# Performance work log

Hardware: AMD Instinct MI355X
Metric: run time of the kernel (lower is better)

The kernel has to match this reference:

```python
import jax, jax.numpy as jnp
import numpy as np

DIM = 256
NUM_HEADS = 8
HEAD_DIM = DIM // NUM_HEADS


def setup_inputs() -> dict:
    key = jax.random.key(0)
    k_x, k_wq, k_bq, k_wp, k_bp = jax.random.split(key, 5)
    B, C, H, W = 2, DIM, 48, 48
    x = jax.random.normal(k_x, (B, C, H, W), dtype=jnp.float32)
    # 1x1 convs are pointwise matmuls: store weights as [out, in]
    w_qkv = jax.random.normal(k_wq, (3 * C, C), dtype=jnp.float32) * (1.0 / np.sqrt(C))
    b_qkv = jax.random.normal(k_bq, (3 * C,), dtype=jnp.float32) * 0.01
    w_proj = jax.random.normal(k_wp, (C, C), dtype=jnp.float32) * (1.0 / np.sqrt(C))
    b_proj = jax.random.normal(k_bp, (C,), dtype=jnp.float32) * 0.01
    return {"x": x, "w_qkv": w_qkv, "b_qkv": b_qkv, "w_proj": w_proj, "b_proj": b_proj}


def reference(x, w_qkv, b_qkv, w_proj, b_proj):
    B, C, H, W = x.shape
    N = H * W
    # qkv 1x1 conv -> pointwise channel matmul
    qkv = jnp.einsum('bchw,oc->bohw', x, w_qkv) + b_qkv[None, :, None, None]
    q, k, v = jnp.split(qkv, 3, axis=1)  # each [B, C, H, W]
    q = q.reshape(B, NUM_HEADS, HEAD_DIM, N)
    k = k.reshape(B, NUM_HEADS, HEAD_DIM, N)
    v = v.reshape(B, NUM_HEADS, HEAD_DIM, N)
    scale = 1.0 / (HEAD_DIM ** 0.5)
    attn = jnp.einsum('bhdn,bhdm->bhnm', q, k) * scale  # [B, H, N, N]
    attn = jax.nn.softmax(attn, axis=-1)
    out = jnp.einsum('bhnm,bhdm->bhdn', attn, v)  # [B, heads, head_dim, N]
    out = out.reshape(B, C, H, W)
    out = jnp.einsum('bchw,oc->bohw', out, w_proj) + b_proj[None, :, None, None]
    return out + x
```

## Files before the change

### kernel.cpp

```cpp
#include <hip/hip_runtime.h>
#include <math.h>

#define C_DIM 256
#define NH 8
#define HD 32
#define BATCH 2
#define NPIX 2304
#define TK 64
#define KP 72

typedef __attribute__((ext_vector_type(8))) short bf16x8;
typedef __attribute__((ext_vector_type(4))) float f32x4;

__device__ __forceinline__ unsigned short f2b(float f) {
    union { float f; unsigned int u; } c; c.f = f;
    unsigned int u = c.u + 0x7FFFu + ((c.u >> 16) & 1u);
    return (unsigned short)(u >> 16);
}

__device__ __forceinline__ unsigned int pk2(float lo, float hi) {
    union { float f; unsigned int u; } a, b;
    a.f = lo; b.f = hi;
    return __builtin_amdgcn_perm(b.u + 0x8000u, a.u + 0x8000u, 0x07060302u);
}

__global__ __launch_bounds__(256) void qkv_gemm(
        const float* __restrict__ x, const float* __restrict__ w,
        const float* __restrict__ bias,
        unsigned short* __restrict__ Qg, unsigned short* __restrict__ Kg,
        unsigned short* __restrict__ Vg)
{
    __shared__ unsigned short a_s[128][KP];
    __shared__ unsigned short b_s[128][KP];

    const int tid  = threadIdx.x;
    const int wv   = tid >> 6;
    const int lane = tid & 63;
    const int l15  = lane & 15;
    const int quad = lane >> 4;
    const int n0   = blockIdx.x * 128;
    const int my   = blockIdx.y;
    const int b    = blockIdx.z;
    const float* xb = x + (size_t)b * C_DIM * NPIX;

    f32x4 acc[8][2];
    #pragma unroll
    for (int i = 0; i < 8; ++i) { acc[i][0] = (f32x4){0,0,0,0}; acc[i][1] = (f32x4){0,0,0,0}; }

    const int ak = (tid & 15) * 4, ai = tid >> 4;
    const int bn = tid & 63,       bk = (tid >> 6) * 16;

    for (int kk = 0; kk < C_DIM; kk += 64) {
        #pragma unroll
        for (int p = 0; p < 8; ++p) {
            const int i = p * 16 + ai;
            const float4 w4 = *(const float4*)(w + (size_t)(my * 128 + i) * C_DIM + kk + ak);
            *(uint2*)&a_s[i][ak] = make_uint2(pk2(w4.x, w4.y), pk2(w4.z, w4.w));
        }
        #pragma unroll
        for (int half = 0; half < 2; ++half) {
            const int n = half * 64 + bn;
            const float* xc = xb + (size_t)(kk + bk) * NPIX + n0 + n;
            #pragma unroll
            for (int t = 0; t < 4; ++t) {
                const float v0 = xc[(size_t)(t * 4 + 0) * NPIX];
                const float v1 = xc[(size_t)(t * 4 + 1) * NPIX];
                const float v2 = xc[(size_t)(t * 4 + 2) * NPIX];
                const float v3 = xc[(size_t)(t * 4 + 3) * NPIX];
                *(uint2*)&b_s[n][bk + t * 4] = make_uint2(pk2(v0, v1), pk2(v2, v3));
            }
        }
        __syncthreads();

        #pragma unroll
        for (int ks = 0; ks < 2; ++ks) {
            bf16x8 bfr[2];
            bfr[0] = *(const bf16x8*)&b_s[wv * 32 + l15][ks * 32 + quad * 8];
            bfr[1] = *(const bf16x8*)&b_s[wv * 32 + 16 + l15][ks * 32 + quad * 8];
            #pragma unroll
            for (int mt = 0; mt < 8; ++mt) {
                const bf16x8 af = *(const bf16x8*)&a_s[mt * 16 + l15][ks * 32 + quad * 8];
                acc[mt][0] = __builtin_amdgcn_mfma_f32_16x16x32_bf16(af, bfr[0], acc[mt][0], 0, 0, 0);
                acc[mt][1] = __builtin_amdgcn_mfma_f32_16x16x32_bf16(af, bfr[1], acc[mt][1], 0, 0, 0);
            }
        }
        __syncthreads();
    }

    const int which = my >> 1;
    #pragma unroll
    for (int mt = 0; mt < 8; ++mt) {
        const int m0 = my * 128 + mt * 16 + quad * 4;
        const float4 b4 = *(const float4*)(bias + m0);
        const int h  = (m0 >> 5) & 7;
        const int d0 = m0 & 31;
        const int bh = b * NH + h;
        #pragma unroll
        for (int nt = 0; nt < 2; ++nt) {
            const int n = n0 + wv * 32 + nt * 16 + l15;
            float v0 = acc[mt][nt][0] + b4.x;
            float v1 = acc[mt][nt][1] + b4.y;
            float v2 = acc[mt][nt][2] + b4.z;
            float v3 = acc[mt][nt][3] + b4.w;
            if (which == 0) {
                const float s = 0.17677669529663687f;
                v0 *= s; v1 *= s; v2 *= s; v3 *= s;
                *(uint2*)&Qg[((size_t)bh * NPIX + n) * HD + d0] =
                    make_uint2(pk2(v0, v1), pk2(v2, v3));
            } else if (which == 1) {
                *(uint2*)&Kg[((size_t)bh * NPIX + n) * HD + d0] =
                    make_uint2(pk2(v0, v1), pk2(v2, v3));
            } else {
                unsigned short* vp = Vg + (size_t)bh * HD * NPIX + (size_t)d0 * NPIX + n;
                vp[0]        = f2b(v0);
                vp[NPIX]     = f2b(v1);
                vp[2 * NPIX] = f2b(v2);
                vp[3 * NPIX] = f2b(v3);
            }
        }
    }
}

#define NT (NPIX / TK)

__global__ __launch_bounds__(256) void attn_kernel(
        const unsigned short* __restrict__ Qg, const unsigned short* __restrict__ Kg,
        const unsigned short* __restrict__ Vg, float* __restrict__ Ot)
{
    __shared__ unsigned short k_s[2][TK][40];
    __shared__ unsigned short v_s[2][HD][76];
    __shared__ unsigned short p_s[4][16][76];
    __shared__ float o_s[HD][68];

    const int tid  = threadIdx.x;
    const int wv   = tid >> 6;
    const int lane = tid & 63;
    const int l15  = lane & 15;
    const int quad = lane >> 4;
    const int bh   = blockIdx.y;
    const int q0   = blockIdx.x * 64;

    const unsigned short* Qh = Qg + (size_t)bh * NPIX * HD;
    const unsigned short* Kh = Kg + (size_t)bh * NPIX * HD;
    const unsigned short* Vh = Vg + (size_t)bh * HD * NPIX;

    const bf16x8 q_frag = *(const bf16x8*)(Qh + (size_t)(q0 + wv * 16 + l15) * HD + quad * 8);

    const int kr = tid >> 2, kc = (tid & 3) * 8;
    const int vd = tid >> 3, vc = (tid & 7) * 8;

    uint4 kreg = *(const uint4*)(Kh + (size_t)kr * HD + kc);
    uint4 vreg = *(const uint4*)(Vh + (size_t)vd * NPIX + vc);
    *(uint4*)&k_s[0][kr][kc] = kreg;
    *(uint4*)&v_s[0][vd][vc] = vreg;

    f32x4 o0 = {0.f, 0.f, 0.f, 0.f};
    f32x4 o1 = {0.f, 0.f, 0.f, 0.f};
    float lsum = 0.f;

    for (int t = 0; t < NT; ++t) {
        const int cur = t & 1;
        if (t + 1 < NT) {
            const int k0 = (t + 1) * TK;
            kreg = *(const uint4*)(Kh + (size_t)(k0 + kr) * HD + kc);
            vreg = *(const uint4*)(Vh + (size_t)vd * NPIX + k0 + vc);
        }
        __syncthreads();

        f32x4 s[4];
        #pragma unroll
        for (int kg = 0; kg < 4; ++kg) {
            const bf16x8 kf = *(const bf16x8*)&k_s[cur][kg * 16 + l15][quad * 8];
            s[kg] = __builtin_amdgcn_mfma_f32_16x16x32_bf16(kf, q_frag,
                        (f32x4){0.f, 0.f, 0.f, 0.f}, 0, 0, 0);
        }

        #pragma unroll
        for (int kg = 0; kg < 4; ++kg) {
            const float p0 = __expf(s[kg][0]);
            const float p1 = __expf(s[kg][1]);
            const float p2 = __expf(s[kg][2]);
            const float p3 = __expf(s[kg][3]);
            lsum += (p0 + p1) + (p2 + p3);
            *(uint2*)&p_s[wv][l15][kg * 16 + quad * 4] =
                make_uint2(pk2(p0, p1), pk2(p2, p3));
        }

        #pragma unroll
        for (int kc2 = 0; kc2 < 2; ++kc2) {
            const bf16x8 pf  = *(const bf16x8*)&p_s[wv][l15][kc2 * 32 + quad * 8];
            const bf16x8 vf0 = *(const bf16x8*)&v_s[cur][l15][kc2 * 32 + quad * 8];
            const bf16x8 vf1 = *(const bf16x8*)&v_s[cur][16 + l15][kc2 * 32 + quad * 8];
            o0 = __builtin_amdgcn_mfma_f32_16x16x32_bf16(vf0, pf, o0, 0, 0, 0);
            o1 = __builtin_amdgcn_mfma_f32_16x16x32_bf16(vf1, pf, o1, 0, 0, 0);
        }

        if (t + 1 < NT) {
            *(uint4*)&k_s[cur ^ 1][kr][kc] = kreg;
            *(uint4*)&v_s[cur ^ 1][vd][vc] = vreg;
        }
    }

    lsum += __shfl_xor(lsum, 16, 64);
    lsum += __shfl_xor(lsum, 32, 64);
    const float inv = 1.f / lsum;

    #pragma unroll
    for (int r = 0; r < 4; ++r) {
        o_s[quad * 4 + r][wv * 16 + l15]      = o0[r] * inv;
        o_s[16 + quad * 4 + r][wv * 16 + l15] = o1[r] * inv;
    }
    __syncthreads();
    const int row = tid >> 3, col = (tid & 7) * 8;
    const int b = bh >> 3, h = bh & 7;
    float* op = Ot + ((size_t)b * C_DIM + h * HD + row) * NPIX + q0 + col;
    *(float4*)op       = *(float4*)&o_s[row][col];
    *((float4*)op + 1) = *(float4*)&o_s[row][col + 4];
}

__global__ __launch_bounds__(256) void proj_gemm(
        const float* __restrict__ A, const float* __restrict__ w,
        const float* __restrict__ bias, const float* __restrict__ x,
        float* __restrict__ out)
{
    __shared__ unsigned short a_s[64][KP];
    __shared__ unsigned short b_s[128][KP];

    const int tid  = threadIdx.x;
    const int wv   = tid >> 6;
    const int lane = tid & 63;
    const int l15  = lane & 15;
    const int quad = lane >> 4;
    const int n0   = blockIdx.x * 128;
    const int my   = blockIdx.y;
    const int b    = blockIdx.z;
    const float* Ab = A + (size_t)b * C_DIM * NPIX;

    f32x4 acc[4][2];
    #pragma unroll
    for (int i = 0; i < 4; ++i) { acc[i][0] = (f32x4){0,0,0,0}; acc[i][1] = (f32x4){0,0,0,0}; }

    const int ak = (tid & 15) * 4, ai = tid >> 4;
    const int bn = tid & 63,       bk = (tid >> 6) * 16;

    for (int kk = 0; kk < C_DIM; kk += 64) {
        #pragma unroll
        for (int p = 0; p < 4; ++p) {
            const int i = p * 16 + ai;
            const float4 w4 = *(const float4*)(w + (size_t)(my * 64 + i) * C_DIM + kk + ak);
            *(uint2*)&a_s[i][ak] = make_uint2(pk2(w4.x, w4.y), pk2(w4.z, w4.w));
        }
        #pragma unroll
        for (int half = 0; half < 2; ++half) {
            const int n = half * 64 + bn;
            const float* xc = Ab + (size_t)(kk + bk) * NPIX + n0 + n;
            #pragma unroll
            for (int t = 0; t < 4; ++t) {
                const float v0 = xc[(size_t)(t * 4 + 0) * NPIX];
                const float v1 = xc[(size_t)(t * 4 + 1) * NPIX];
                const float v2 = xc[(size_t)(t * 4 + 2) * NPIX];
                const float v3 = xc[(size_t)(t * 4 + 3) * NPIX];
                *(uint2*)&b_s[n][bk + t * 4] = make_uint2(pk2(v0, v1), pk2(v2, v3));
            }
        }
        __syncthreads();

        #pragma unroll
        for (int ks = 0; ks < 2; ++ks) {
            bf16x8 bfr[2];
            bfr[0] = *(const bf16x8*)&b_s[wv * 32 + l15][ks * 32 + quad * 8];
            bfr[1] = *(const bf16x8*)&b_s[wv * 32 + 16 + l15][ks * 32 + quad * 8];
            #pragma unroll
            for (int mt = 0; mt < 4; ++mt) {
                const bf16x8 af = *(const bf16x8*)&a_s[mt * 16 + l15][ks * 32 + quad * 8];
                acc[mt][0] = __builtin_amdgcn_mfma_f32_16x16x32_bf16(af, bfr[0], acc[mt][0], 0, 0, 0);
                acc[mt][1] = __builtin_amdgcn_mfma_f32_16x16x32_bf16(af, bfr[1], acc[mt][1], 0, 0, 0);
            }
        }
        __syncthreads();
    }

    #pragma unroll
    for (int mt = 0; mt < 4; ++mt) {
        const int m0 = my * 64 + mt * 16 + quad * 4;
        const float4 b4 = *(const float4*)(bias + m0);
        #pragma unroll
        for (int nt = 0; nt < 2; ++nt) {
            const int n = n0 + wv * 32 + nt * 16 + l15;
            const size_t base = ((size_t)b * C_DIM + m0) * NPIX + n;
            out[base]            = acc[mt][nt][0] + b4.x + x[base];
            out[base + NPIX]     = acc[mt][nt][1] + b4.y + x[base + NPIX];
            out[base + 2 * NPIX] = acc[mt][nt][2] + b4.z + x[base + 2 * NPIX];
            out[base + 3 * NPIX] = acc[mt][nt][3] + b4.w + x[base + 3 * NPIX];
        }
    }
}

extern "C" void kernel_launch(void* const* d_in, const int* in_sizes, int n_in,
                              void* d_out, int out_size, void* d_ws, size_t ws_size,
                              hipStream_t stream)
{
    const float* x      = (const float*)d_in[0];
    const float* w_qkv  = (const float*)d_in[1];
    const float* b_qkv  = (const float*)d_in[2];
    const float* w_proj = (const float*)d_in[3];
    const float* b_proj = (const float*)d_in[4];
    float* out = (float*)d_out;

    const size_t TSZ = (size_t)BATCH * NH * NPIX * HD;
    unsigned short* Qg = (unsigned short*)d_ws;
    unsigned short* Kg = Qg + TSZ;
    unsigned short* Vg = Qg + 2 * TSZ;
    float* Ot = (float*)(Qg + 3 * TSZ);

    qkv_gemm<<<dim3(18, 6, 2), 256, 0, stream>>>(x, w_qkv, b_qkv, Qg, Kg, Vg);
    attn_kernel<<<dim3(36, 16), 256, 0, stream>>>(Qg, Kg, Vg, Ot);
    proj_gemm<<<dim3(18, 4, 2), 256, 0, stream>>>(Ot, w_proj, b_proj, x, out);
}
```

Measured before the change: 121.8 us.

## Shrink GEMM tiles and double-buffer LDS with register prefetch in both 1x1-conv GEMMs

Both pointwise GEMM kernels move to smaller output tiles (64x64 for qkv, 32x64 for proj), which gives 4x more blocks so more CUs are occupied. The global loads for the next K slice are prefetched into registers and written to a second LDS buffer while MFMAs run on the current buffer, leaving one barrier per step instead of two. The attention grid is transposed so that consecutive blocks cover different heads. Smaller tiles mean less reuse per loaded element and more redundant weight and activation traffic.

```diff
diff --git a/kernel.cpp b/kernel.cpp
--- a/kernel.cpp
+++ b/kernel.cpp
@@ -30,93 +30,108 @@
         unsigned short* __restrict__ Qg, unsigned short* __restrict__ Kg,
         unsigned short* __restrict__ Vg)
 {
-    __shared__ unsigned short a_s[128][KP];
-    __shared__ unsigned short b_s[128][KP];
+    __shared__ unsigned short a_s[2][64][KP];
+    __shared__ unsigned short b_s[2][64][KP];
 
     const int tid  = threadIdx.x;
     const int wv   = tid >> 6;
     const int lane = tid & 63;
     const int l15  = lane & 15;
     const int quad = lane >> 4;
-    const int n0   = blockIdx.x * 128;
+    const int n0   = blockIdx.x * 64;
     const int my   = blockIdx.y;
     const int b    = blockIdx.z;
     const float* xb = x + (size_t)b * C_DIM * NPIX;
 
-    f32x4 acc[8][2];
-    #pragma unroll
-    for (int i = 0; i < 8; ++i) { acc[i][0] = (f32x4){0,0,0,0}; acc[i][1] = (f32x4){0,0,0,0}; }
+    f32x4 acc[4];
+    #pragma unroll
+    for (int i = 0; i < 4; ++i) acc[i] = (f32x4){0.f, 0.f, 0.f, 0.f};
 
     const int ak = (tid & 15) * 4, ai = tid >> 4;
     const int bn = tid & 63,       bk = (tid >> 6) * 16;
 
-    for (int kk = 0; kk < C_DIM; kk += 64) {
-        #pragma unroll
-        for (int p = 0; p < 8; ++p) {
-            const int i = p * 16 + ai;
-            const float4 w4 = *(const float4*)(w + (size_t)(my * 128 + i) * C_DIM + kk + ak);
-            *(uint2*)&a_s[i][ak] = make_uint2(pk2(w4.x, w4.y), pk2(w4.z, w4.w));
-        }
-        #pragma unroll
-        for (int half = 0; half < 2; ++half) {
-            const int n = half * 64 + bn;
-            const float* xc = xb + (size_t)(kk + bk) * NPIX + n0 + n;
-            #pragma unroll
-            for (int t = 0; t < 4; ++t) {
-                const float v0 = xc[(size_t)(t * 4 + 0) * NPIX];
-                const float v1 = xc[(size_t)(t * 4 + 1) * NPIX];
-                const float v2 = xc[(size_t)(t * 4 + 2) * NPIX];
-                const float v3 = xc[(size_t)(t * 4 + 3) * NPIX];
-                *(uint2*)&b_s[n][bk + t * 4] = make_uint2(pk2(v0, v1), pk2(v2, v3));
+    float4 aw[4];
+    float  bw[16];
+
+    #pragma unroll
+    for (int p = 0; p < 4; ++p)
+        aw[p] = *(const float4*)(w + (size_t)(my * 64 + p * 16 + ai) * C_DIM + ak);
+    {
+        const float* xc = xb + (size_t)bk * NPIX + n0 + bn;
+        #pragma unroll
+        for (int t = 0; t < 16; ++t) bw[t] = xc[(size_t)t * NPIX];
+    }
+    #pragma unroll
+    for (int p = 0; p < 4; ++p)
+        *(uint2*)&a_s[0][p * 16 + ai][ak] =
+            make_uint2(pk2(aw[p].x, aw[p].y), pk2(aw[p].z, aw[p].w));
+    #pragma unroll
+    for (int t = 0; t < 4; ++t)
+        *(uint2*)&b_s[0][bn][bk + t * 4] =
+            make_uint2(pk2(bw[t*4], bw[t*4+1]), pk2(bw[t*4+2], bw[t*4+3]));
+
+    #pragma unroll
+    for (int step = 0; step < 4; ++step) {
+        const int cur = step & 1;
+        if (step < 3) {
+            const int kk = (step + 1) * 64;
+            #pragma unroll
+            for (int p = 0; p < 4; ++p)
+                aw[p] = *(const float4*)(w + (size_t)(my * 64 + p * 16 + ai) * C_DIM + kk + ak);
+            const float* xc = xb + (size_t)(kk + bk) * NPIX + n0 + bn;
+            #pragma unroll
+            for (int t = 0; t < 16; ++t) bw[t] = xc[(size_t)t * NPIX];
+        }
+        __syncthreads();
+
+        #pragma unroll
+        for (int ks = 0; ks < 2; ++ks) {
+            const bf16x8 bfr = *(const bf16x8*)&b_s[cur][wv * 16 + l15][ks * 32 + quad * 8];
+            #pragma unroll
+            for (int mt = 0; mt < 4; ++mt) {
+                const bf16x8 af = *(const bf16x8*)&a_s[cur][mt * 16 + l15][ks * 32 + quad * 8];
+                acc[mt] = __builtin_amdgcn_mfma_f32_16x16x32_bf16(af, bfr, acc[mt], 0, 0, 0);
             }
         }
-        __syncthreads();
-
-        #pragma unroll
-        for (int ks = 0; ks < 2; ++ks) {
-            bf16x8 bfr[2];
-            bfr[0] = *(const bf16x8*)&b_s[wv * 32 + l15][ks * 32 + quad * 8];
-            bfr[1] = *(const bf16x8*)&b_s[wv * 32 + 16 + l15][ks * 32 + quad * 8];
-            #pragma unroll
-            for (int mt = 0; mt < 8; ++mt) {
-                const bf16x8 af = *(const bf16x8*)&a_s[mt * 16 + l15][ks * 32 + quad * 8];
-                acc[mt][0] = __builtin_amdgcn_mfma_f32_16x16x32_bf16(af, bfr[0], acc[mt][0], 0, 0, 0);
-                acc[mt][1] = __builtin_amdgcn_mfma_f32_16x16x32_bf16(af, bfr[1], acc[mt][1], 0, 0, 0);
-            }
-        }
-        __syncthreads();
-    }
-
-    const int which = my >> 1;
-    #pragma unroll
-    for (int mt = 0; mt < 8; ++mt) {
-        const int m0 = my * 128 + mt * 16 + quad * 4;
+        if (step < 3) {
+            #pragma unroll
+            for (int p = 0; p < 4; ++p)
+                *(uint2*)&a_s[cur ^ 1][p * 16 + ai][ak] =
+                    make_uint2(pk2(aw[p].x, aw[p].y), pk2(aw[p].z, aw[p].w));
+            #pragma unroll
+            for (int t = 0; t < 4; ++t)
+                *(uint2*)&b_s[cur ^ 1][bn][bk + t * 4] =
+                    make_uint2(pk2(bw[t*4], bw[t*4+1]), pk2(bw[t*4+2], bw[t*4+3]));
+        }
+    }
+
+    const int which = my >> 2;
+    #pragma unroll
+    for (int mt = 0; mt < 4; ++mt) {
+        const int m0 = my * 64 + mt * 16 + quad * 4;
         const float4 b4 = *(const float4*)(bias + m0);
         const int h  = (m0 >> 5) & 7;
         const int d0 = m0 & 31;
         const int bh = b * NH + h;
-        #pragma unroll
-        for (int nt = 0; nt < 2; ++nt) {
-            const int n = n0 + wv * 32 + nt * 16 + l15;
-            float v0 = acc[mt][nt][0] + b4.x;
-            float v1 = acc[mt][nt][1] + b4.y;
-            float v2 = acc[mt][nt][2] + b4.z;
-            float v3 = acc[mt][nt][3] + b4.w;
-            if (which == 0) {
-                const float s = 0.17677669529663687f;
-                v0 *= s; v1 *= s; v2 *= s; v3 *= s;
-                *(uint2*)&Qg[((size_t)bh * NPIX + n) * HD + d0] =
-                    make_uint2(pk2(v0, v1), pk2(v2, v3));
-            } else if (which == 1) {
-                *(uint2*)&Kg[((size_t)bh * NPIX + n) * HD + d0] =
-                    make_uint2(pk2(v0, v1), pk2(v2, v3));
-            } else {
-                unsigned short* vp = Vg + (size_t)bh * HD * NPIX + (size_t)d0 * NPIX + n;
-                vp[0]        = f2b(v0);
-                vp[NPIX]     = f2b(v1);
-                vp[2 * NPIX] = f2b(v2);
-                vp[3 * NPIX] = f2b(v3);
-            }
+        const int n  = n0 + wv * 16 + l15;
+        float v0 = acc[mt][0] + b4.x;
+        float v1 = acc[mt][1] + b4.y;
+        float v2 = acc[mt][2] + b4.z;
+        float v3 = acc[mt][3] + b4.w;
+        if (which == 0) {
+            const float s = 0.17677669529663687f;
+            v0 *= s; v1 *= s; v2 *= s; v3 *= s;
+            *(uint2*)&Qg[((size_t)bh * NPIX + n) * HD + d0] =
+                make_uint2(pk2(v0, v1), pk2(v2, v3));
+        } else if (which == 1) {
+            *(uint2*)&Kg[((size_t)bh * NPIX + n) * HD + d0] =
+                make_uint2(pk2(v0, v1), pk2(v2, v3));
+        } else {
+            unsigned short* vp = Vg + (size_t)bh * HD * NPIX + (size_t)d0 * NPIX + n;
+            vp[0]        = f2b(v0);
+            vp[NPIX]     = f2b(v1);
+            vp[2 * NPIX] = f2b(v2);
+            vp[3 * NPIX] = f2b(v3);
         }
     }
 }
@@ -137,8 +152,8 @@
     const int lane = tid & 63;
     const int l15  = lane & 15;
     const int quad = lane >> 4;
-    const int bh   = blockIdx.y;
-    const int q0   = blockIdx.x * 64;
+    const int bh   = blockIdx.x;
+    const int q0   = blockIdx.y * 64;
 
     const unsigned short* Qh = Qg + (size_t)bh * NPIX * HD;
     const unsigned short* Kh = Kg + (size_t)bh * NPIX * HD;
@@ -223,76 +238,91 @@
         const float* __restrict__ bias, const float* __restrict__ x,
         float* __restrict__ out)
 {
-    __shared__ unsigned short a_s[64][KP];
-    __shared__ unsigned short b_s[128][KP];
+    __shared__ unsigned short a_s[2][32][KP];
+    __shared__ unsigned short b_s[2][64][KP];
 
     const int tid  = threadIdx.x;
     const int wv   = tid >> 6;
     const int lane = tid & 63;
     const int l15  = lane & 15;
     const int quad = lane >> 4;
-    const int n0   = blockIdx.x * 128;
+    const int n0   = blockIdx.x * 64;
     const int my   = blockIdx.y;
     const int b    = blockIdx.z;
     const float* Ab = A + (size_t)b * C_DIM * NPIX;
 
-    f32x4 acc[4][2];
-    #pragma unroll
-    for (int i = 0; i < 4; ++i) { acc[i][0] = (f32x4){0,0,0,0}; acc[i][1] = (f32x4){0,0,0,0}; }
+    f32x4 acc[2];
+    acc[0] = (f32x4){0.f, 0.f, 0.f, 0.f};
+    acc[1] = (f32x4){0.f, 0.f, 0.f, 0.f};
 
     const int ak = (tid & 15) * 4, ai = tid >> 4;
     const int bn = tid & 63,       bk = (tid >> 6) * 16;
 
-    for (int kk = 0; kk < C_DIM; kk += 64) {
-        #pragma unroll
-        for (int p = 0; p < 4; ++p) {
-            const int i = p * 16 + ai;
-            const float4 w4 = *(const float4*)(w + (size_t)(my * 64 + i) * C_DIM + kk + ak);
-            *(uint2*)&a_s[i][ak] = make_uint2(pk2(w4.x, w4.y), pk2(w4.z, w4.w));
-        }
-        #pragma unroll
-        for (int half = 0; half < 2; ++half) {
-            const int n = half * 64 + bn;
-            const float* xc = Ab + (size_t)(kk + bk) * NPIX + n0 + n;
-            #pragma unroll
-            for (int t = 0; t < 4; ++t) {
-                const float v0 = xc[(size_t)(t * 4 + 0) * NPIX];
-                const float v1 = xc[(size_t)(t * 4 + 1) * NPIX];
-                const float v2 = xc[(size_t)(t * 4 + 2) * NPIX];
-                const float v3 = xc[(size_t)(t * 4 + 3) * NPIX];
-                *(uint2*)&b_s[n][bk + t * 4] = make_uint2(pk2(v0, v1), pk2(v2, v3));
+    float4 aw[2];
+    float  bw[16];
+
+    #pragma unroll
+    for (int p = 0; p < 2; ++p)
+        aw[p] = *(const float4*)(w + (size_t)(my * 32 + p * 16 + ai) * C_DIM + ak);
+    {
+        const float* xc = Ab + (size_t)bk * NPIX + n0 + bn;
+        #pragma unroll
+        for (int t = 0; t < 16; ++t) bw[t] = xc[(size_t)t * NPIX];
+    }
+    #pragma unroll
+    for (int p = 0; p < 2; ++p)
+        *(uint2*)&a_s[0][p * 16 + ai][ak] =
+            make_uint2(pk2(aw[p].x, aw[p].y), pk2(aw[p].z, aw[p].w));
+    #pragma unroll
+    for (int t = 0; t < 4; ++t)
+        *(uint2*)&b_s[0][bn][bk + t * 4] =
+            make_uint2(pk2(bw[t*4], bw[t*4+1]), pk2(bw[t*4+2], bw[t*4+3]));
+
+    #pragma unroll
+    for (int step = 0; step < 4; ++step) {
+        const int cur = step & 1;
+        if (step < 3) {
+            const int kk = (step + 1) * 64;
+            #pragma unroll
+            for (int p = 0; p < 2; ++p)
+                aw[p] = *(const float4*)(w + (size_t)(my * 32 + p * 16 + ai) * C_DIM + kk + ak);
+            const float* xc = Ab + (size_t)(kk + bk) * NPIX + n0 + bn;
+            #pragma unroll
+            for (int t = 0; t < 16; ++t) bw[t] = xc[(size_t)t * NPIX];
+        }
+        __syncthreads();
+
+        #pragma unroll
+        for (int ks = 0; ks < 2; ++ks) {
+            const bf16x8 bfr = *(const bf16x8*)&b_s[cur][wv * 16 + l15][ks * 32 + quad * 8];
+            #pragma unroll
+            for (int mt = 0; mt < 2; ++mt) {
+                const bf16x8 af = *(const bf16x8*)&a_s[cur][mt * 16 + l15][ks * 32 + quad * 8];
+                acc[mt] = __builtin_amdgcn_mfma_f32_16x16x32_bf16(af, bfr, acc[mt], 0, 0, 0);
             }
         }
-        __syncthreads();
-
-        #pragma unroll
-        for (int ks = 0; ks < 2; ++ks) {
-            bf16x8 bfr[2];
-            bfr[0] = *(const bf16x8*)&b_s[wv * 32 + l15][ks * 32 + quad * 8];
-            bfr[1] = *(const bf16x8*)&b_s[wv * 32 + 16 + l15][ks * 32 + quad * 8];
-            #pragma unroll
-            for (int mt = 0; mt < 4; ++mt) {
-                const bf16x8 af = *(const bf16x8*)&a_s[mt * 16 + l15][ks * 32 + quad * 8];
-                acc[mt][0] = __builtin_amdgcn_mfma_f32_16x16x32_bf16(af, bfr[0], acc[mt][0], 0, 0, 0);
-                acc[mt][1] = __builtin_amdgcn_mfma_f32_16x16x32_bf16(af, bfr[1], acc[mt][1], 0, 0, 0);
-            }
-        }
-        __syncthreads();
-    }
-
-    #pragma unroll
-    for (int mt = 0; mt < 4; ++mt) {
-        const int m0 = my * 64 + mt * 16 + quad * 4;
+        if (step < 3) {
+            #pragma unroll
+            for (int p = 0; p < 2; ++p)
+                *(uint2*)&a_s[cur ^ 1][p * 16 + ai][ak] =
+                    make_uint2(pk2(aw[p].x, aw[p].y), pk2(aw[p].z, aw[p].w));
+            #pragma unroll
+            for (int t = 0; t < 4; ++t)
+                *(uint2*)&b_s[cur ^ 1][bn][bk + t * 4] =
+                    make_uint2(pk2(bw[t*4], bw[t*4+1]), pk2(bw[t*4+2], bw[t*4+3]));
+        }
+    }
+
+    #pragma unroll
+    for (int mt = 0; mt < 2; ++mt) {
+        const int m0 = my * 32 + mt * 16 + quad * 4;
         const float4 b4 = *(const float4*)(bias + m0);
-        #pragma unroll
-        for (int nt = 0; nt < 2; ++nt) {
-            const int n = n0 + wv * 32 + nt * 16 + l15;
-            const size_t base = ((size_t)b * C_DIM + m0) * NPIX + n;
-            out[base]            = acc[mt][nt][0] + b4.x + x[base];
-            out[base + NPIX]     = acc[mt][nt][1] + b4.y + x[base + NPIX];
-            out[base + 2 * NPIX] = acc[mt][nt][2] + b4.z + x[base + 2 * NPIX];
-            out[base + 3 * NPIX] = acc[mt][nt][3] + b4.w + x[base + 3 * NPIX];
-        }
+        const int n = n0 + wv * 16 + l15;
+        const size_t base = ((size_t)b * C_DIM + m0) * NPIX + n;
+        out[base]            = acc[mt][0] + b4.x + x[base];
+        out[base + NPIX]     = acc[mt][1] + b4.y + x[base + NPIX];
+        out[base + 2 * NPIX] = acc[mt][2] + b4.z + x[base + 2 * NPIX];
+        out[base + 3 * NPIX] = acc[mt][3] + b4.w + x[base + 3 * NPIX];
     }
 }
 
@@ -313,7 +343,7 @@
     unsigned short* Vg = Qg + 2 * TSZ;
     float* Ot = (float*)(Qg + 3 * TSZ);
 
-    qkv_gemm<<<dim3(18, 6, 2), 256, 0, stream>>>(x, w_qkv, b_qkv, Qg, Kg, Vg);
-    attn_kernel<<<dim3(36, 16), 256, 0, stream>>>(Qg, Kg, Vg, Ot);
-    proj_gemm<<<dim3(18, 4, 2), 256, 0, stream>>>(Ot, w_proj, b_proj, x, out);
-}
+    qkv_gemm<<<dim3(36, 12, 2), 256, 0, stream>>>(x, w_qkv, b_qkv, Qg, Kg, Vg);
+    attn_kernel<<<dim3(16, 36), 256, 0, stream>>>(Qg, Kg, Vg, Ot);
+    proj_gemm<<<dim3(36, 8, 2), 256, 0, stream>>>(Ot, w_proj, b_proj, x, out);
+}
```

Measured after the change: 118.2 us. 1.03x faster.

## Pre-pack inputs and weights into MFMA fragment layout, drop LDS staging in GEMMs

Applied to the files above, without the earlier changes.

Adds prep kernels that convert x and both weight matrices to bf16 in an MFMA-fragment-ordered layout. The QKV and projection GEMMs then load fragments straight from global memory with no LDS staging or K-loop syncs. Their epilogues go through per-wave LDS so global stores are coalesced. The attention kernel now writes its output as bf16 in the same packed layout and uses a swapped grid order. The aim is to cut strided fp32 loads and conversion work inside the GEMMs and halve attention-output traffic, at the cost of two extra kernel launches and an extra pass over x.

```diff
diff --git a/kernel.cpp b/kernel.cpp
--- a/kernel.cpp
+++ b/kernel.cpp
@@ -7,138 +7,162 @@
 #define BATCH 2
 #define NPIX 2304
 #define TK 64
-#define KP 72
+#define NGRP (NPIX / 16)
 
 typedef __attribute__((ext_vector_type(8))) short bf16x8;
 typedef __attribute__((ext_vector_type(4))) float f32x4;
+
+#define OFF_XT  0u
+#define OFF_Q   1179648u
+#define OFF_K   2359296u
+#define OFF_V   3538944u
+#define OFF_OT  4718592u
+#define OFF_WQ  5898240u
+#define OFF_WP  6094848u
 
 __device__ __forceinline__ unsigned short f2b(float f) {
     union { float f; unsigned int u; } c; c.f = f;
     unsigned int u = c.u + 0x7FFFu + ((c.u >> 16) & 1u);
     return (unsigned short)(u >> 16);
 }
-
 __device__ __forceinline__ unsigned int pk2(float lo, float hi) {
     union { float f; unsigned int u; } a, b;
     a.f = lo; b.f = hi;
     return __builtin_amdgcn_perm(b.u + 0x8000u, a.u + 0x8000u, 0x07060302u);
 }
 
+__global__ __launch_bounds__(256) void prep_xt(
+        const float* __restrict__ x, unsigned short* __restrict__ xT)
+{
+    __shared__ unsigned short t_s[64][72];
+    const int tid = threadIdx.x;
+    const int n0 = blockIdx.x * 64, c0 = blockIdx.y * 64, b = blockIdx.z;
+    const int nl = tid & 63, cq = tid >> 6;
+    #pragma unroll
+    for (int p = 0; p < 8; ++p) {
+        const int c = p * 8 + cq * 2;
+        const float f0 = x[((size_t)b * C_DIM + c0 + c) * NPIX + n0 + nl];
+        const float f1 = x[((size_t)b * C_DIM + c0 + c + 1) * NPIX + n0 + nl];
+        *(unsigned int*)&t_s[nl][c] = pk2(f0, f1);
+    }
+    __syncthreads();
+    const int row = tid >> 2, jq = tid & 3;
+    #pragma unroll
+    for (int hh = 0; hh < 2; ++hh) {
+        const int jl = jq * 2 + hh;
+        const int jg = blockIdx.y * 8 + jl;
+        const int ngrp = blockIdx.x * 4 + (row >> 4);
+        unsigned short* dst = xT + (((size_t)b * NGRP + ngrp) * 32 + jg) * 128 + (row & 15) * 8;
+        *(uint4*)dst = *(uint4*)&t_s[row][jl * 8];
+    }
+}
+
+__global__ __launch_bounds__(256) void prep_w(
+        const float* __restrict__ wqkv, const float* __restrict__ wproj,
+        unsigned short* __restrict__ wq, unsigned short* __restrict__ wp)
+{
+    const int t = blockIdx.x * 256 + threadIdx.x;
+    const float* src; unsigned short* dst;
+    if (t < 24576) {
+        const int m = t >> 5, j = t & 31;
+        src = wqkv + ((size_t)m * C_DIM + j * 8);
+        dst = wq + ((size_t)((m >> 4) * 32 + j) * 16 + (m & 15)) * 8;
+    } else {
+        const int t2 = t - 24576, m = t2 >> 5, j = t2 & 31;
+        src = wproj + ((size_t)m * C_DIM + j * 8);
+        dst = wp + ((size_t)((m >> 4) * 32 + j) * 16 + (m & 15)) * 8;
+    }
+    const float4 f0 = *(const float4*)src, f1 = *(const float4*)(src + 4);
+    *(uint4*)dst = make_uint4(pk2(f0.x, f0.y), pk2(f0.z, f0.w),
+                              pk2(f1.x, f1.y), pk2(f1.z, f1.w));
+}
+
 __global__ __launch_bounds__(256) void qkv_gemm(
-        const float* __restrict__ x, const float* __restrict__ w,
+        const unsigned short* __restrict__ xT, const unsigned short* __restrict__ wq,
         const float* __restrict__ bias,
         unsigned short* __restrict__ Qg, unsigned short* __restrict__ Kg,
         unsigned short* __restrict__ Vg)
 {
-    __shared__ unsigned short a_s[128][KP];
-    __shared__ unsigned short b_s[128][KP];
+    __shared__ unsigned short eplds[4][2560];
+    const int tid = threadIdx.x, wv = tid >> 6, lane = tid & 63;
+    const int l15 = lane & 15, quad = lane >> 4;
+    const int n0 = blockIdx.x * 256, my = blockIdx.y, b = blockIdx.z;
+    const int nw = n0 + wv * 64;
+
+    bf16x8 af[8];
+    #pragma unroll
+    for (int kc = 0; kc < 8; ++kc)
+        af[kc] = *(const bf16x8*)(wq + ((size_t)(my * 32 + kc * 4 + quad) * 16 + l15) * 8);
+
+    f32x4 acc[4];
+    #pragma unroll
+    for (int i = 0; i < 4; ++i) acc[i] = (f32x4){0.f, 0.f, 0.f, 0.f};
+
+    #pragma unroll
+    for (int sub = 0; sub < 4; ++sub) {
+        const int ngrp = (nw + sub * 16) >> 4;
+        const unsigned short* bp = xT + ((size_t)b * NGRP + ngrp) * 32 * 128;
+        #pragma unroll
+        for (int kc = 0; kc < 8; ++kc) {
+            const bf16x8 bf = *(const bf16x8*)(bp + (size_t)(kc * 4 + quad) * 128 + l15 * 8);
+            acc[sub] = __builtin_amdgcn_mfma_f32_16x16x32_bf16(af[kc], bf, acc[sub], 0, 0, 0);
+        }
+    }
+
+    const int which = my >> 4;
+    const int ch0 = (my & 15) * 16;
+    const int h = ch0 >> 5, d0 = ch0 & 31, bh = b * NH + h;
+    const float4 b4 = *(const float4*)(bias + my * 16 + quad * 4);
+    unsigned short* wl = eplds[wv];
+
+    if (which < 2) {
+        const float sc = (which == 0) ? 0.17677669529663687f : 1.0f;
+        #pragma unroll
+        for (int sub = 0; sub < 4; ++sub) {
+            const float v0 = (acc[sub][0] + b4.x) * sc, v1 = (acc[sub][1] + b4.y) * sc;
+            const float v2 = (acc[sub][2] + b4.z) * sc, v3 = (acc[sub][3] + b4.w) * sc;
+            *(uint2*)&wl[(sub * 16 + l15) * 40 + quad * 4] =
+                make_uint2(pk2(v0, v1), pk2(v2, v3));
+        }
+        unsigned short* dst = ((which == 0) ? Qg : Kg)
+                            + ((size_t)bh * NPIX + nw + lane) * HD + d0;
+        *(uint4*)dst       = *(uint4*)&wl[lane * 40];
+        *(uint4*)(dst + 8) = *(uint4*)&wl[lane * 40 + 8];
+    } else {
+        #pragma unroll
+        for (int sub = 0; sub < 4; ++sub) {
+            wl[(quad * 4 + 0) * 72 + sub * 16 + l15] = f2b(acc[sub][0] + b4.x);
+            wl[(quad * 4 + 1) * 72 + sub * 16 + l15] = f2b(acc[sub][1] + b4.y);
+            wl[(quad * 4 + 2) * 72 + sub * 16 + l15] = f2b(acc[sub][2] + b4.z);
+            wl[(quad * 4 + 3) * 72 + sub * 16 + l15] = f2b(acc[sub][3] + b4.w);
+        }
+        #pragma unroll
+        for (int p = 0; p < 2; ++p) {
+            const int row = p * 8 + (lane >> 3), cn = (lane & 7) * 8;
+            *(uint4*)(Vg + ((size_t)bh * HD + d0 + row) * NPIX + nw + cn) =
+                *(uint4*)&wl[row * 72 + cn];
+        }
+    }
+}
+
+#define NT (NPIX / TK)
+
+__global__ __launch_bounds__(256) void attn_kernel(
+        const unsigned short* __restrict__ Qg, const unsigned short* __restrict__ Kg,
+        const unsigned short* __restrict__ Vg, unsigned short* __restrict__ OtT)
+{
+    __shared__ unsigned short k_s[2][TK][40];
+    __shared__ unsigned short v_s[2][HD][76];
+    __shared__ unsigned short p_s[4][16][76];
+    __shared__ unsigned short o_sT[64][40];
 
     const int tid  = threadIdx.x;
     const int wv   = tid >> 6;
     const int lane = tid & 63;
     const int l15  = lane & 15;
     const int quad = lane >> 4;
-    const int n0   = blockIdx.x * 128;
-    const int my   = blockIdx.y;
-    const int b    = blockIdx.z;
-    const float* xb = x + (size_t)b * C_DIM * NPIX;
-
-    f32x4 acc[8][2];
-    #pragma unroll
-    for (int i = 0; i < 8; ++i) { acc[i][0] = (f32x4){0,0,0,0}; acc[i][1] = (f32x4){0,0,0,0}; }
-
-    const int ak = (tid & 15) * 4, ai = tid >> 4;
-    const int bn = tid & 63,       bk = (tid >> 6) * 16;
-
-    for (int kk = 0; kk < C_DIM; kk += 64) {
-        #pragma unroll
-        for (int p = 0; p < 8; ++p) {
-            const int i = p * 16 + ai;
-            const float4 w4 = *(const float4*)(w + (size_t)(my * 128 + i) * C_DIM + kk + ak);
-            *(uint2*)&a_s[i][ak] = make_uint2(pk2(w4.x, w4.y), pk2(w4.z, w4.w));
-        }
-        #pragma unroll
-        for (int half = 0; half < 2; ++half) {
-            const int n = half * 64 + bn;
-            const float* xc = xb + (size_t)(kk + bk) * NPIX + n0 + n;
-            #pragma unroll
-            for (int t = 0; t < 4; ++t) {
-                const float v0 = xc[(size_t)(t * 4 + 0) * NPIX];
-                const float v1 = xc[(size_t)(t * 4 + 1) * NPIX];
-                const float v2 = xc[(size_t)(t * 4 + 2) * NPIX];
-                const float v3 = xc[(size_t)(t * 4 + 3) * NPIX];
-                *(uint2*)&b_s[n][bk + t * 4] = make_uint2(pk2(v0, v1), pk2(v2, v3));
-            }
-        }
-        __syncthreads();
-
-        #pragma unroll
-        for (int ks = 0; ks < 2; ++ks) {
-            bf16x8 bfr[2];
-            bfr[0] = *(const bf16x8*)&b_s[wv * 32 + l15][ks * 32 + quad * 8];
-            bfr[1] = *(const bf16x8*)&b_s[wv * 32 + 16 + l15][ks * 32 + quad * 8];
-            #pragma unroll
-            for (int mt = 0; mt < 8; ++mt) {
-                const bf16x8 af = *(const bf16x8*)&a_s[mt * 16 + l15][ks * 32 + quad * 8];
-                acc[mt][0] = __builtin_amdgcn_mfma_f32_16x16x32_bf16(af, bfr[0], acc[mt][0], 0, 0, 0);
-                acc[mt][1] = __builtin_amdgcn_mfma_f32_16x16x32_bf16(af, bfr[1], acc[mt][1], 0, 0, 0);
-            }
-        }
-        __syncthreads();
-    }
-
-    const int which = my >> 1;
-    #pragma unroll
-    for (int mt = 0; mt < 8; ++mt) {
-        const int m0 = my * 128 + mt * 16 + quad * 4;
-        const float4 b4 = *(const float4*)(bias + m0);
-        const int h  = (m0 >> 5) & 7;
-        const int d0 = m0 & 31;
-        const int bh = b * NH + h;
-        #pragma unroll
-        for (int nt = 0; nt < 2; ++nt) {
-            const int n = n0 + wv * 32 + nt * 16 + l15;
-            float v0 = acc[mt][nt][0] + b4.x;
-            float v1 = acc[mt][nt][1] + b4.y;
-            float v2 = acc[mt][nt][2] + b4.z;
-            float v3 = acc[mt][nt][3] + b4.w;
-            if (which == 0) {
-                const float s = 0.17677669529663687f;
-                v0 *= s; v1 *= s; v2 *= s; v3 *= s;
-                *(uint2*)&Qg[((size_t)bh * NPIX + n) * HD + d0] =
-                    make_uint2(pk2(v0, v1), pk2(v2, v3));
-            } else if (which == 1) {
-                *(uint2*)&Kg[((size_t)bh * NPIX + n) * HD + d0] =
-                    make_uint2(pk2(v0, v1), pk2(v2, v3));
-            } else {
-                unsigned short* vp = Vg + (size_t)bh * HD * NPIX + (size_t)d0 * NPIX + n;
-                vp[0]        = f2b(v0);
-                vp[NPIX]     = f2b(v1);
-                vp[2 * NPIX] = f2b(v2);
-                vp[3 * NPIX] = f2b(v3);
-            }
-        }
-    }
-}
-
-#define NT (NPIX / TK)
-
-__global__ __launch_bounds__(256) void attn_kernel(
-        const unsigned short* __restrict__ Qg, const unsigned short* __restrict__ Kg,
-        const unsigned short* __restrict__ Vg, float* __restrict__ Ot)
-{
-    __shared__ unsigned short k_s[2][TK][40];
-    __shared__ unsigned short v_s[2][HD][76];
-    __shared__ unsigned short p_s[4][16][76];
-    __shared__ float o_s[HD][68];
-
-    const int tid  = threadIdx.x;
-    const int wv   = tid >> 6;
-    const int lane = tid & 63;
-    const int l15  = lane & 15;
-    const int quad = lane >> 4;
-    const int bh   = blockIdx.y;
-    const int q0   = blockIdx.x * 64;
+    const int bh   = blockIdx.x;
+    const int q0   = blockIdx.y * 64;
 
     const unsigned short* Qh = Qg + (size_t)bh * NPIX * HD;
     const unsigned short* Kh = Kg + (size_t)bh * NPIX * HD;
@@ -205,94 +229,71 @@
     lsum += __shfl_xor(lsum, 32, 64);
     const float inv = 1.f / lsum;
 
-    #pragma unroll
-    for (int r = 0; r < 4; ++r) {
-        o_s[quad * 4 + r][wv * 16 + l15]      = o0[r] * inv;
-        o_s[16 + quad * 4 + r][wv * 16 + l15] = o1[r] * inv;
-    }
+    *(uint2*)&o_sT[wv * 16 + l15][quad * 4] =
+        make_uint2(pk2(o0[0] * inv, o0[1] * inv), pk2(o0[2] * inv, o0[3] * inv));
+    *(uint2*)&o_sT[wv * 16 + l15][16 + quad * 4] =
+        make_uint2(pk2(o1[0] * inv, o1[1] * inv), pk2(o1[2] * inv, o1[3] * inv));
     __syncthreads();
-    const int row = tid >> 3, col = (tid & 7) * 8;
+    const int row = tid >> 2, jq = tid & 3;
     const int b = bh >> 3, h = bh & 7;
-    float* op = Ot + ((size_t)b * C_DIM + h * HD + row) * NPIX + q0 + col;
-    *(float4*)op       = *(float4*)&o_s[row][col];
-    *((float4*)op + 1) = *(float4*)&o_s[row][col + 4];
+    const int q = q0 + row;
+    unsigned short* dst = OtT + (((size_t)b * NGRP + (q >> 4)) * 32 + h * 4 + jq) * 128
+                        + (q & 15) * 8;
+    *(uint4*)dst = *(uint4*)&o_sT[row][jq * 8];
 }
 
 __global__ __launch_bounds__(256) void proj_gemm(
-        const float* __restrict__ A, const float* __restrict__ w,
+        const unsigned short* __restrict__ OtT, const unsigned short* __restrict__ wp,
         const float* __restrict__ bias, const float* __restrict__ x,
         float* __restrict__ out)
 {
-    __shared__ unsigned short a_s[64][KP];
-    __shared__ unsigned short b_s[128][KP];
-
-    const int tid  = threadIdx.x;
-    const int wv   = tid >> 6;
-    const int lane = tid & 63;
-    const int l15  = lane & 15;
-    const int quad = lane >> 4;
-    const int n0   = blockIdx.x * 128;
-    const int my   = blockIdx.y;
-    const int b    = blockIdx.z;
-    const float* Ab = A + (size_t)b * C_DIM * NPIX;
-
-    f32x4 acc[4][2];
-    #pragma unroll
-    for (int i = 0; i < 4; ++i) { acc[i][0] = (f32x4){0,0,0,0}; acc[i][1] = (f32x4){0,0,0,0}; }
-
-    const int ak = (tid & 15) * 4, ai = tid >> 4;
-    const int bn = tid & 63,       bk = (tid >> 6) * 16;
-
-    for (int kk = 0; kk < C_DIM; kk += 64) {
-        #pragma unroll
-        for (int p = 0; p < 4; ++p) {
-            const int i = p * 16 + ai;
-            const float4 w4 = *(const float4*)(w + (size_t)(my * 64 + i) * C_DIM + kk + ak);
-            *(uint2*)&a_s[i][ak] = make_uint2(pk2(w4.x, w4.y), pk2(w4.z, w4.w));
-        }
-        #pragma unroll
-        for (int half = 0; half < 2; ++half) {
-            const int n = half * 64 + bn;
-            const float* xc = Ab + (size_t)(kk + bk) * NPIX + n0 + n;
-            #pragma unroll
-            for (int t = 0; t < 4; ++t) {
-                const float v0 = xc[(size_t)(t * 4 + 0) * NPIX];
-                const float v1 = xc[(size_t)(t * 4 + 1) * NPIX];
-                const float v2 = xc[(size_t)(t * 4 + 2) * NPIX];
-                const float v3 = xc[(size_t)(t * 4 + 3) * NPIX];
-                *(uint2*)&b_s[n][bk + t * 4] = make_uint2(pk2(v0, v1), pk2(v2, v3));
-            }
-        }
-        __syncthreads();
-
-        #pragma unroll
-        for (int ks = 0; ks < 2; ++ks) {
-            bf16x8 bfr[2];
-            bfr[0] = *(const bf16x8*)&b_s[wv * 32 + l15][ks * 32 + quad * 8];
-            bfr[1] = *(const bf16x8*)&b_s[wv * 32 + 16 + l15][ks * 32 + quad * 8];
-            #pragma unroll
-            for (int mt = 0; mt < 4; ++mt) {
-                const bf16x8 af = *(const bf16x8*)&a_s[mt * 16 + l15][ks * 32 + quad * 8];
-                acc[mt][0] = __builtin_amdgcn_mfma_f32_16x16x32_bf16(af, bfr[0], acc[mt][0], 0, 0, 0);
-                acc[mt][1] = __builtin_amdgcn_mfma_f32_16x16x32_bf16(af, bfr[1], acc[mt][1], 0, 0, 0);
-            }
-        }
-        __syncthreads();
-    }
-
-    #pragma unroll
-    for (int mt = 0; mt < 4; ++mt) {
-        const int m0 = my * 64 + mt * 16 + quad * 4;
-        const float4 b4 = *(const float4*)(bias + m0);
-        #pragma unroll
-        for (int nt = 0; nt < 2; ++nt) {
-            const int n = n0 + wv * 32 + nt * 16 + l15;
-            const size_t base = ((size_t)b * C_DIM + m0) * NPIX + n;
-            out[base]            = acc[mt][nt][0] + b4.x + x[base];
-            out[base + NPIX]     = acc[mt][nt][1] + b4.y + x[base + NPIX];
-            out[base + 2 * NPIX] = acc[mt][nt][2] + b4.z + x[base + 2 * NPIX];
-            out[base + 3 * NPIX] = acc[mt][nt][3] + b4.w + x[base + 3 * NPIX];
-        }
+    __shared__ float plds[4][576];
+    const int tid = threadIdx.x, wv = tid >> 6, lane = tid & 63;
+    const int l15 = lane & 15, quad = lane >> 4;
+    const int n0 = blockIdx.x * 128, my = blockIdx.y, b = blockIdx.z;
+    const int nw = n0 + wv * 32;
+
+    bf16x8 af[8];
+    #pragma unroll
+    for (int kc = 0; kc < 8; ++kc)
+        af[kc] = *(const bf16x8*)(wp + ((size_t)(my * 32 + kc * 4 + quad) * 16 + l15) * 8);
+
+    f32x4 acc[2];
+    acc[0] = (f32x4){0.f, 0.f, 0.f, 0.f};
+    acc[1] = (f32x4){0.f, 0.f, 0.f, 0.f};
+
+    #pragma unroll
+    for (int sub = 0; sub < 2; ++sub) {
+        const int ngrp = (nw + sub * 16) >> 4;
+        const unsigned short* bp = OtT + ((size_t)b * NGRP + ngrp) * 32 * 128;
+        #pragma unroll
+        for (int kc = 0; kc < 8; ++kc) {
+            const bf16x8 bf = *(const bf16x8*)(bp + (size_t)(kc * 4 + quad) * 128 + l15 * 8);
+            acc[sub] = __builtin_amdgcn_mfma_f32_16x16x32_bf16(af[kc], bf, acc[sub], 0, 0, 0);
+        }
+    }
+
+    float* wl = plds[wv];
+    #pragma unroll
+    for (int sub = 0; sub < 2; ++sub) {
+        wl[(quad * 4 + 0) * 36 + sub * 16 + l15] = acc[sub][0];
+        wl[(quad * 4 + 1) * 36 + sub * 16 + l15] = acc[sub][1];
+        wl[(quad * 4 + 2) * 36 + sub * 16 + l15] = acc[sub][2];
+        wl[(quad * 4 + 3) * 36 + sub * 16 + l15] = acc[sub][3];
+    }
+    const int m0 = my * 16;
+    #pragma unroll
+    for (int p = 0; p < 2; ++p) {
+        const int row = p * 8 + (lane >> 3), cn = (lane & 7) * 4;
+        const int c = m0 + row;
+        const size_t idx = ((size_t)b * C_DIM + c) * NPIX + nw + cn;
+        const f32x4 v = *(const f32x4*)&wl[row * 36 + cn];
+        const f32x4 r = *(const f32x4*)(x + idx);
+        const float bv = bias[c];
+        f32x4 o;
+        o[0] = v[0] + bv + r[0]; o[1] = v[1] + bv + r[1];
+        o[2] = v[2] + bv + r[2]; o[3] = v[3] + bv + r[3];
+        *(f32x4*)(out + idx) = o;
     }
 }
 
@@ -307,13 +308,18 @@
     const float* b_proj = (const float*)d_in[4];
     float* out = (float*)d_out;
 
-    const size_t TSZ = (size_t)BATCH * NH * NPIX * HD;
-    unsigned short* Qg = (unsigned short*)d_ws;
-    unsigned short* Kg = Qg + TSZ;
-    unsigned short* Vg = Qg + 2 * TSZ;
-    float* Ot = (float*)(Qg + 3 * TSZ);
-
-    qkv_gemm<<<dim3(18, 6, 2), 256, 0, stream>>>(x, w_qkv, b_qkv, Qg, Kg, Vg);
-    attn_kernel<<<dim3(36, 16), 256, 0, stream>>>(Qg, Kg, Vg, Ot);
-    proj_gemm<<<dim3(18, 4, 2), 256, 0, stream>>>(Ot, w_proj, b_proj, x, out);
-}
+    unsigned short* ws = (unsigned short*)d_ws;
+    unsigned short* xT  = ws + OFF_XT;
+    unsigned short* Qg  = ws + OFF_Q;
+    unsigned short* Kg  = ws + OFF_K;
+    unsigned short* Vg  = ws + OFF_V;
+    unsigned short* OtT = ws + OFF_OT;
+    unsigned short* wq  = ws + OFF_WQ;
+    unsigned short* wp  = ws + OFF_WP;
+
+    prep_xt<<<dim3(36, 4, 2), 256, 0, stream>>>(x, xT);
+    prep_w<<<dim3(128), 256, 0, stream>>>(w_qkv, w_proj, wq, wp);
+    qkv_gemm<<<dim3(9, 48, 2), 256, 0, stream>>>(xT, wq, b_qkv, Qg, Kg, Vg);
+    attn_kernel<<<dim3(16, 36), 256, 0, stream>>>(Qg, Kg, Vg, OtT);
+    proj_gemm<<<dim3(18, 16, 2), 256, 0, stream>>>(OtT, wp, b_proj, x, out);
+}
```

Measured after the change: 120.8 us. About the same (-0.8%).
